# Performance work log

Measured on AMD Instinct MI355X. Metric: run time of the kernel, lower is better.

The kernel has to match this reference:

```python
import jax, jax.numpy as jnp
import numpy as np

NF = 32      # feature channels
DG = 4       # deformable groups
K = 9        # 3x3 kernel taps


def _conv(x, w, b, stride=1):
    # x: [B,C,H,W], w: [O,I,3,3] (pad=1)
    y = jax.lax.conv_general_dilated(x, w, (stride, stride), ((1, 1), (1, 1)),
                                     dimension_numbers=('NCHW', 'OIHW', 'NCHW'))
    return y + b[None, :, None, None]


def _lrelu(x):
    return jnp.where(x >= 0, x, 0.1 * x)


def _up2(x):
    # bilinear, align_corners=False (half-pixel centers, matches torch F.interpolate)
    B, C, H, W = x.shape
    return jax.image.resize(x, (B, C, 2 * H, 2 * W), method='bilinear')


def _deform_conv(x, om, w, b):
    # Modulated deformable conv (DCNv2), stride=1, pad=1, dilation=1, 3x3.
    # x: [B,C,H,W]; om: [B,3*DG*K,H,W] = (offset_y | offset_x | mask) blocks.
    B, C, H, W = x.shape
    Cg = C // DG
    o1, o2, m = jnp.split(om, 3, axis=1)
    off_y = o1.reshape(B, DG, K, H, W)
    off_x = o2.reshape(B, DG, K, H, W)
    mask = jax.nn.sigmoid(m).reshape(B, DG, K, H, W)
    k = jnp.arange(K)
    dy = (k // 3 - 1).astype(x.dtype)            # kernel tap y displacement
    dx = (k % 3 - 1).astype(x.dtype)
    # sampling positions [B,DG,K,H,W]
    py = off_y + jnp.arange(H, dtype=x.dtype)[:, None] + dy[:, None, None]
    px = off_x + jnp.arange(W, dtype=x.dtype)[None, :] + dx[:, None, None]
    y0 = jnp.floor(py)
    x0 = jnp.floor(px)
    wy1 = py - y0
    wx1 = px - x0
    y0i = y0.astype(jnp.int32)
    x0i = x0.astype(jnp.int32)
    imgf = x.reshape(B, DG, Cg, H * W)

    def corner(yi, xi, wt):
        valid = (yi >= 0) & (yi < H) & (xi >= 0) & (xi < W)
        yc = jnp.clip(yi, 0, H - 1)
        xc = jnp.clip(xi, 0, W - 1)
        idx = (yc * W + xc).reshape(B, DG, 1, K * H * W)
        v = jnp.take_along_axis(imgf, idx, axis=3).reshape(B, DG, Cg, K, H, W)
        return v * (wt * valid)[:, :, None]

    samp = (corner(y0i, x0i, (1 - wy1) * (1 - wx1))
            + corner(y0i, x0i + 1, (1 - wy1) * wx1)
            + corner(y0i + 1, x0i, wy1 * (1 - wx1))
            + corner(y0i + 1, x0i + 1, wy1 * wx1))
    samp = samp * mask[:, :, None]                       # [B,DG,Cg,K,H,W]
    out = jnp.einsum('bgckhw,ogck->bohw', samp, w.reshape(w.shape[0], DG, Cg, K))
    return out + b[None, :, None, None]


_PARAM_SHAPES = [
    ('w1_1', (32, 64, 3, 3)), ('b1_1', (32,)),
    ('w2_1', (32, 32, 3, 3)), ('b2_1', (32,)),
    ('w3_1', (32, 32, 3, 3)), ('b3_1', (32,)),
    ('w4_1', (32, 32, 3, 3)), ('b4_1', (32,)),
    ('w6_1', (32, 32, 3, 3)), ('b6_1', (32,)),
    ('w7_1', (32, 32, 3, 3)), ('b7_1', (32,)),
    ('w1_2', (32, 64, 3, 3)), ('b1_2', (32,)),
    ('w2_2', (32, 32, 3, 3)), ('b2_2', (32,)),
    ('w3_2', (32, 64, 3, 3)), ('b3_2', (32,)),
    ('w4_2', (32, 32, 3, 3)), ('b4_2', (32,)),
    ('w_om', (108, 32, 3, 3)), ('b_om', (108,)),   # DCN_sep conv_offset_mask: 3*DG*K=108
    ('w_dcn', (32, 32, 3, 3)), ('b_dcn', (32,)),
]


def setup_inputs() -> dict:
    key = jax.random.key(0)
    ks = jax.random.split(key, len(_PARAM_SHAPES) + 2)
    B, H, W = 4, 192, 192
    d = {
        'fea1': jax.random.normal(ks[0], (B, NF, H, W), jnp.float32),
        'fea2': jax.random.normal(ks[1], (B, NF, H, W), jnp.float32),
    }
    for i, (name, shp) in enumerate(_PARAM_SHAPES):
        d[name] = jax.random.normal(ks[i + 2], shp, jnp.float32) * 0.05
    return d


def reference(fea1, fea2, w1_1, b1_1, w2_1, b2_1, w3_1, b3_1, w4_1, b4_1,
              w6_1, b6_1, w7_1, b7_1, w1_2, b1_2, w2_2, b2_2, w3_2, b3_2,
              w4_2, b4_2, w_om, b_om, w_dcn, b_dcn):
    off = _lrelu(_conv(jnp.concatenate([fea1, fea2], 1), w1_1, b1_1))
    off1 = _lrelu(_conv(off, w2_1, b2_1))
    off2 = _lrelu(_conv(off1, w3_1, b3_1, 2))   # H/2
    off2 = _lrelu(_conv(off2, w4_1, b4_1))
    off3 = _lrelu(_conv(off2, w6_1, b6_1, 2))   # H/4
    off3 = _lrelu(_conv(off3, w7_1, b7_1))
    up = _up2(off3)                              # back to H/2
    off = _lrelu(_conv(jnp.concatenate([up, off2], 1), w1_2, b1_2))
    off = _lrelu(_conv(off, w2_2, b2_2))
    up = _up2(off)                               # back to H
    off = _lrelu(_conv(jnp.concatenate([up, off1], 1), w3_2, b3_2))
    base_offset = _conv(off, w4_2, b4_2)
    om = _conv(base_offset, w_om, b_om)          # DCN_sep offset/mask head
    return _deform_conv(fea2, om, w_dcn, b_dcn)
```

## Files before the change

kernel.cpp:

```cpp
#include <hip/hip_runtime.h>
#include <math.h>


#define BDIM 256

typedef __attribute__((ext_vector_type(8))) short short8v;
typedef __attribute__((ext_vector_type(4))) float f32x4;

__device__ __forceinline__ unsigned short f2bf(float f) {
    unsigned u = __builtin_bit_cast(unsigned, f);
    u = (u + 0x7FFF + ((u >> 16) & 1)) >> 16;
    return (unsigned short)u;
}
__device__ __forceinline__ float bf2f(unsigned short h) {
    unsigned u = ((unsigned)h) << 16;
    return __builtin_bit_cast(float, u);
}

template<int NPASS, int NHALF, int STRIDE, bool LRELU>
__global__ __launch_bounds__(BDIM, 4)
void convm_k(const short* __restrict__ in0, const short* __restrict__ in1,
             const short* __restrict__ wf,
             const float* __restrict__ bias,
             short* __restrict__ out,
             int Hin, int Win, int Hout, int Wout, int OCS)
{
    const int lane = threadIdx.x & 63;
    const int wid  = blockIdx.x * 4 + (threadIdx.x >> 6);
    const int segs = Wout >> 4;
    const int b  = wid / (Hout * segs);
    int r = wid - b * (Hout * segs);
    const int oy = r / segs;
    const int x0 = (r - oy * segs) * 16;
    const int lp = lane & 15;
    const int g  = lane >> 4;

    int rowOff[3]; bool rowOk[3];
#pragma unroll
    for (int ty = 0; ty < 3; ++ty) {
        const int iy = oy * STRIDE + ty - 1;
        rowOk[ty] = (unsigned)iy < (unsigned)Hin;
        rowOff[ty] = min(max(iy, 0), Hin - 1) * Win;
    }
    int colOff[3]; bool colOk[3];
#pragma unroll
    for (int tx = 0; tx < 3; ++tx) {
        const int ix = (x0 + lp) * STRIDE + tx - 1;
        colOk[tx] = (unsigned)ix < (unsigned)Win;
        colOff[tx] = min(max(ix, 0), Win - 1) * 32 + g * 8;
    }

    f32x4 acc[NHALF];
#pragma unroll
    for (int h = 0; h < NHALF; ++h) acc[h] = (f32x4){0.f, 0.f, 0.f, 0.f};

    const size_t inPlane = (size_t)Hin * Win * 32;
    const short8v zero = {};

#pragma unroll
    for (int pass = 0; pass < NPASS; ++pass) {
        const short* inp = (pass == 0 ? in0 : in1) + (size_t)b * inPlane;

        short8v bv[9];
#pragma unroll
        for (int t = 0; t < 9; ++t) {
            const int ty = t / 3, tx = t % 3;
            short8v v = *(const short8v*)(inp + (size_t)rowOff[ty] * 32 + colOff[tx]);
            bv[t] = (rowOk[ty] & colOk[tx]) ? v : zero;
        }
#pragma unroll
        for (int t = 0; t < 9; ++t) {
#pragma unroll
            for (int h = 0; h < NHALF; ++h) {
                short8v av = *(const short8v*)(
                    wf + ((((size_t)pass * 9 + t) * NHALF + h) * 64 + lane) * 8);
                acc[h] = __builtin_amdgcn_mfma_f32_16x16x32_bf16(av, bv[t], acc[h], 0, 0, 0);
            }
        }
    }

    short* op = out + (((size_t)b * Hout + oy) * Wout + x0 + lp) * OCS;
#pragma unroll
    for (int h = 0; h < NHALF; ++h) {
        const int co0 = h * 16 + g * 4;
        ushort4 st;
#pragma unroll
        for (int j = 0; j < 4; ++j) {
            float v = acc[h][j] + bias[co0 + j];
            if (LRELU) v = (v >= 0.f) ? v : 0.1f * v;
            ((unsigned short*)&st)[j] = f2bf(v);
        }
        *(ushort4*)(op + co0) = st;
    }
}

struct WPArgs {
    const float* src[11];
    int off[11];
    int npass[11], nhalf[11], O[11];
};

__global__ __launch_bounds__(BDIM)
void wprep_k(WPArgs a, short* __restrict__ wbase)
{
    const int z = blockIdx.z;
    const int n = a.npass[z] * 9 * a.nhalf[z] * 512;
    const int idx = blockIdx.x * BDIM + threadIdx.x;
    if (idx >= n) return;
    const int j = idx & 7;
    const int l = (idx >> 3) & 63;
    int r = idx >> 9;
    const int h = r % a.nhalf[z]; r /= a.nhalf[z];
    const int t = r % 9;
    const int pass = r / 9;
    const int I = a.npass[z] * 32;
    const int cout = h * 16 + (l & 15);
    const int cin  = pass * 32 + (l >> 4) * 8 + j;
    float v = (cout < a.O[z]) ? a.src[z][((size_t)cout * I + cin) * 9 + t] : 0.f;
    wbase[a.off[z] + idx] = (short)f2bf(v);
}

__global__ __launch_bounds__(BDIM)
void wdp_k(const float* __restrict__ w, short* __restrict__ dst)
{
    const int idx = blockIdx.x * BDIM + threadIdx.x;
    if (idx >= 9 * 2 * 64 * 8) return;
    const int j = idx & 7;
    const int l = (idx >> 3) & 63;
    const int h = (idx >> 9) & 1;
    const int k = idx >> 10;
    const int cout = h * 16 + (l & 15);
    const int cin  = (l >> 4) * 8 + j;
    dst[idx] = (short)f2bf(w[((size_t)cout * 32 + cin) * 9 + k]);
}

__global__ __launch_bounds__(BDIM)
void cvtnhwc_k(const float* __restrict__ s0, const float* __restrict__ s1,
               short* __restrict__ d0, short* __restrict__ d1, int H, int W)
{
    const float* s = blockIdx.z ? s1 : s0;
    short* d = blockIdx.z ? d1 : d0;
    const int idx = blockIdx.x * BDIM + threadIdx.x;
    if (idx >= 4 * 32 * H * W) return;
    const int c = idx & 31;
    int t = idx >> 5;
    const int x = t % W; t /= W;
    const int y = t % H;
    const int b = t / H;
    d[idx] = (short)f2bf(s[(((size_t)b * 32 + c) * H + y) * W + x]);
}

__global__ __launch_bounds__(BDIM)
void up2b_k(const short* __restrict__ in, short* __restrict__ out,
            int Hin, int Win)
{
    const int Hout = 2 * Hin, Wout = 2 * Win;
    const int idx = blockIdx.x * BDIM + threadIdx.x;
    if (idx >= 4 * Hout * Wout * 4) return;
    const int cg = idx & 3;
    int t = idx >> 2;
    const int x = t % Wout; t /= Wout;
    const int y = t % Hout;
    const int b = t / Hout;

    const float sy = (y + 0.5f) * 0.5f - 0.5f;
    const float sx = (x + 0.5f) * 0.5f - 0.5f;
    const float y0f = floorf(sy), x0f = floorf(sx);
    const float wy = sy - y0f, wx = sx - x0f;
    const int y0 = (int)y0f, x0 = (int)x0f;
    const int y0c = min(max(y0, 0), Hin - 1);
    const int y1c = min(max(y0 + 1, 0), Hin - 1);
    const int x0c = min(max(x0, 0), Win - 1);
    const int x1c = min(max(x0 + 1, 0), Win - 1);

    const short* base = in + (size_t)b * Hin * Win * 32 + cg * 8;
    short8v v00 = *(const short8v*)(base + ((size_t)y0c * Win + x0c) * 32);
    short8v v01 = *(const short8v*)(base + ((size_t)y0c * Win + x1c) * 32);
    short8v v10 = *(const short8v*)(base + ((size_t)y1c * Win + x0c) * 32);
    short8v v11 = *(const short8v*)(base + ((size_t)y1c * Win + x1c) * 32);

    short8v o;
#pragma unroll
    for (int j = 0; j < 8; ++j) {
        float f = (1.f - wy) * ((1.f - wx) * bf2f((unsigned short)v00[j]) +
                                wx * bf2f((unsigned short)v01[j]))
                + wy * ((1.f - wx) * bf2f((unsigned short)v10[j]) +
                        wx * bf2f((unsigned short)v11[j]));
        o[j] = (short)f2bf(f);
    }
    short* op = out + (size_t)b * Hout * Wout * 32 + ((size_t)y * Wout + x) * 32 + cg * 8;
    *(short8v*)op = o;
}

__global__ __launch_bounds__(BDIM, 4)
void dcnm_k(const short* __restrict__ xb,
            const short* __restrict__ bo,
            const short* __restrict__ wfo,
            const float* __restrict__ obias,
            const short* __restrict__ wfd,
            const float* __restrict__ bias,
            float* __restrict__ out, int H, int W)
{
    __shared__ unsigned short omld[4][16][112];

    const int lane = threadIdx.x & 63;
    const int wv   = threadIdx.x >> 6;
    const int wid  = blockIdx.x * 4 + wv;
    const int segs = W >> 4;
    const int b = wid / (H * segs);
    int r = wid - b * (H * segs);
    const int y = r / segs;
    const int x0 = (r - y * segs) * 16;
    const int lp = lane & 15;
    const int g  = lane >> 4;
    const int x  = x0 + lp;
    const size_t plane = (size_t)H * W;
    const short8v zero = {};

    {
        int rowOff[3]; bool rowOk[3];
#pragma unroll
        for (int ty = 0; ty < 3; ++ty) {
            const int iy = y + ty - 1;
            rowOk[ty] = (unsigned)iy < (unsigned)H;
            rowOff[ty] = min(max(iy, 0), H - 1) * W;
        }
        int colOff[3]; bool colOk[3];
#pragma unroll
        for (int tx = 0; tx < 3; ++tx) {
            const int ix = x + tx - 1;
            colOk[tx] = (unsigned)ix < (unsigned)W;
            colOff[tx] = min(max(ix, 0), W - 1) * 32 + g * 8;
        }
        const short* inp = bo + (size_t)b * plane * 32;
        short8v bv[9];
#pragma unroll
        for (int t = 0; t < 9; ++t) {
            const int ty = t / 3, tx = t % 3;
            short8v v = *(const short8v*)(inp + (size_t)rowOff[ty] * 32 + colOff[tx]);
            bv[t] = (rowOk[ty] & colOk[tx]) ? v : zero;
        }
        f32x4 acc[7];
#pragma unroll
        for (int h = 0; h < 7; ++h) acc[h] = (f32x4){0.f, 0.f, 0.f, 0.f};
#pragma unroll
        for (int t = 0; t < 9; ++t) {
#pragma unroll
            for (int h = 0; h < 7; ++h) {
                short8v av = *(const short8v*)(wfo + (((size_t)t * 7 + h) * 64 + lane) * 8);
                acc[h] = __builtin_amdgcn_mfma_f32_16x16x32_bf16(av, bv[t], acc[h], 0, 0, 0);
            }
        }
#pragma unroll
        for (int h = 0; h < 7; ++h) {
            const int co0 = h * 16 + g * 4;
            ushort4 st;
#pragma unroll
            for (int j = 0; j < 4; ++j)
                ((unsigned short*)&st)[j] = f2bf(acc[h][j] + obias[min(co0 + j, 107)]);
            *(ushort4*)&omld[wv][lp][co0] = st;
        }
    }
    __syncthreads();

    f32x4 p0 = (f32x4){0.f, 0.f, 0.f, 0.f};
    f32x4 p1 = (f32x4){0.f, 0.f, 0.f, 0.f};
    const short* xbb = xb + (size_t)b * plane * 32 + g * 8;

#pragma unroll
    for (int k = 0; k < 9; ++k) {
        const float offy = bf2f(omld[wv][lp][g * 9 + k]);
        const float offx = bf2f(omld[wv][lp][36 + g * 9 + k]);
        const float ml   = bf2f(omld[wv][lp][72 + g * 9 + k]);
        const float m = 1.f / (1.f + __expf(-ml));

        const float py = offy + (float)y + (float)(k / 3 - 1);
        const float px = offx + (float)x + (float)(k % 3 - 1);
        const float y0f = floorf(py), x0f = floorf(px);
        const int y0 = (int)y0f, x0i = (int)x0f;
        const float wy1 = py - y0f, wx1 = px - x0f;
        const float wy0 = 1.f - wy1, wx0 = 1.f - wx1;

        const bool y0ok = (unsigned)y0 < (unsigned)H;
        const bool y1ok = (unsigned)(y0 + 1) < (unsigned)H;
        const bool x0ok = (unsigned)x0i < (unsigned)W;
        const bool x1ok = (unsigned)(x0i + 1) < (unsigned)W;
        const int y0c = min(max(y0, 0), H - 1);
        const int y1c = min(max(y0 + 1, 0), H - 1);
        const int x0c = min(max(x0i, 0), W - 1);
        const int x1c = min(max(x0i + 1, 0), W - 1);

        const float w00 = wy0 * wx0 * ((y0ok && x0ok) ? 1.f : 0.f) * m;
        const float w01 = wy0 * wx1 * ((y0ok && x1ok) ? 1.f : 0.f) * m;
        const float w10 = wy1 * wx0 * ((y1ok && x0ok) ? 1.f : 0.f) * m;
        const float w11 = wy1 * wx1 * ((y1ok && x1ok) ? 1.f : 0.f) * m;

        short8v v00 = *(const short8v*)(xbb + ((size_t)y0c * W + x0c) * 32);
        short8v v01 = *(const short8v*)(xbb + ((size_t)y0c * W + x1c) * 32);
        short8v v10 = *(const short8v*)(xbb + ((size_t)y1c * W + x0c) * 32);
        short8v v11 = *(const short8v*)(xbb + ((size_t)y1c * W + x1c) * 32);

        short8v bv;
#pragma unroll
        for (int j = 0; j < 8; ++j) {
            float s = w00 * bf2f((unsigned short)v00[j])
                    + w01 * bf2f((unsigned short)v01[j])
                    + w10 * bf2f((unsigned short)v10[j])
                    + w11 * bf2f((unsigned short)v11[j]);
            bv[j] = (short)f2bf(s);
        }

        short8v a0 = *(const short8v*)(wfd + (((size_t)k * 2 + 0) * 64 + lane) * 8);
        short8v a1 = *(const short8v*)(wfd + (((size_t)k * 2 + 1) * 64 + lane) * 8);
        p0 = __builtin_amdgcn_mfma_f32_16x16x32_bf16(a0, bv, p0, 0, 0, 0);
        p1 = __builtin_amdgcn_mfma_f32_16x16x32_bf16(a1, bv, p1, 0, 0, 0);
    }

    float* op = out + (size_t)b * 32 * plane + (size_t)y * W + x;
#pragma unroll
    for (int j = 0; j < 4; ++j) {
        const int co0 = g * 4 + j;
        const int co1 = 16 + g * 4 + j;
        op[(size_t)co0 * plane] = p0[j] + bias[co0];
        op[(size_t)co1 * plane] = p1[j] + bias[co1];
    }
}


extern "C" void kernel_launch(void* const* d_in, const int* in_sizes, int n_in,
                              void* d_out, int out_size, void* d_ws, size_t ws_size,
                              hipStream_t stream)
{
    const float* fea1  = (const float*)d_in[0];
    const float* fea2  = (const float*)d_in[1];
    const float* w1_1  = (const float*)d_in[2];  const float* b1_1 = (const float*)d_in[3];
    const float* w2_1  = (const float*)d_in[4];  const float* b2_1 = (const float*)d_in[5];
    const float* w3_1  = (const float*)d_in[6];  const float* b3_1 = (const float*)d_in[7];
    const float* w4_1  = (const float*)d_in[8];  const float* b4_1 = (const float*)d_in[9];
    const float* w6_1  = (const float*)d_in[10]; const float* b6_1 = (const float*)d_in[11];
    const float* w7_1  = (const float*)d_in[12]; const float* b7_1 = (const float*)d_in[13];
    const float* w1_2  = (const float*)d_in[14]; const float* b1_2 = (const float*)d_in[15];
    const float* w2_2  = (const float*)d_in[16]; const float* b2_2 = (const float*)d_in[17];
    const float* w3_2  = (const float*)d_in[18]; const float* b3_2 = (const float*)d_in[19];
    const float* w4_2  = (const float*)d_in[20]; const float* b4_2 = (const float*)d_in[21];
    const float* w_om  = (const float*)d_in[22]; const float* b_om = (const float*)d_in[23];
    const float* w_dcn = (const float*)d_in[24]; const float* b_dcn= (const float*)d_in[25];

    const int H = 192, W = 192;
    char* ws = (char*)d_ws;

    short* fea1b = (short*)(ws + 0);
    short* fea2b = (short*)(ws + 9437184);
    short* bufA  = (short*)(ws + 18874368);
    short* bufB  = (short*)(ws + 28311552);
    short* bufC  = (short*)(ws + 0);
    short* bufD  = (short*)(ws + 2359296);
    short* bufE  = (short*)(ws + 4718592);
    short* bufF  = (short*)(ws + 5308416);
    short* bufG  = (short*)(ws + 5898240);
    short* bufH  = (short*)(ws + 0);
    short* bufI  = (short*)(ws + 4718592);
    short* bufJ  = (short*)(ws + 37748736);
    short* bufK  = (short*)(ws + 18874368);
    short* bufL  = (short*)(ws + 0);
    short* wfrag = (short*)(ws + 70778880);
    short* wfdcn = (short*)(ws + 71083008);

    const int WOFF[11] = {0, 18432, 27648, 36864, 46080, 55296,
                          64512, 82944, 92160, 110592, 119808};

    dim3 blk(BDIM, 1, 1);

    {
        WPArgs a;
        const float* srcs[11] = {w1_1, w2_1, w3_1, w4_1, w6_1, w7_1,
                                 w1_2, w2_2, w3_2, w4_2, w_om};
        const int NP[11] = {2,1,1,1,1,1,2,1,2,1,1};
        const int NH[11] = {2,2,2,2,2,2,2,2,2,2,7};
        const int Os[11] = {32,32,32,32,32,32,32,32,32,32,108};
        for (int i = 0; i < 11; ++i) {
            a.src[i] = srcs[i]; a.off[i] = WOFF[i];
            a.npass[i] = NP[i]; a.nhalf[i] = NH[i]; a.O[i] = Os[i];
        }
        wprep_k<<<dim3(126, 1, 11), blk, 0, stream>>>(a, wfrag);
        cvtnhwc_k<<<dim3(18432, 1, 2), blk, 0, stream>>>(fea1, fea2, fea1b, fea2b, H, W);
        wdp_k<<<dim3(36), blk, 0, stream>>>(w_dcn, wfdcn);
    }

    convm_k<2,2,1,true><<<dim3(2304), blk, 0, stream>>>(
        fea1b, fea2b, wfrag + WOFF[0], b1_1, bufA, 192,192,192,192, 32);
    convm_k<1,2,1,true><<<dim3(2304), blk, 0, stream>>>(
        bufA, nullptr, wfrag + WOFF[1], b2_1, bufB, 192,192,192,192, 32);
    convm_k<1,2,2,true><<<dim3(576), blk, 0, stream>>>(
        bufB, nullptr, wfrag + WOFF[2], b3_1, bufC, 192,192,96,96, 32);
    convm_k<1,2,1,true><<<dim3(576), blk, 0, stream>>>(
        bufC, nullptr, wfrag + WOFF[3], b4_1, bufD, 96,96,96,96, 32);
    convm_k<1,2,2,true><<<dim3(144), blk, 0, stream>>>(
        bufD, nullptr, wfrag + WOFF[4], b6_1, bufE, 96,96,48,48, 32);
    convm_k<1,2,1,true><<<dim3(144), blk, 0, stream>>>(
        bufE, nullptr, wfrag + WOFF[5], b7_1, bufF, 48,48,48,48, 32);
    up2b_k<<<dim3(576), blk, 0, stream>>>(bufF, bufG, 48, 48);
    convm_k<2,2,1,true><<<dim3(576), blk, 0, stream>>>(
        bufG, bufD, wfrag + WOFF[6], b1_2, bufH, 96,96,96,96, 32);
    convm_k<1,2,1,true><<<dim3(576), blk, 0, stream>>>(
        bufH, nullptr, wfrag + WOFF[7], b2_2, bufI, 96,96,96,96, 32);
    up2b_k<<<dim3(2304), blk, 0, stream>>>(bufI, bufJ, 96, 96);
    convm_k<2,2,1,true><<<dim3(2304), blk, 0, stream>>>(
        bufJ, bufB, wfrag + WOFF[8], b3_2, bufK, 192,192,192,192, 32);
    convm_k<1,2,1,false><<<dim3(2304), blk, 0, stream>>>(
        bufK, nullptr, wfrag + WOFF[9], b4_2, bufL, 192,192,192,192, 32);
    dcnm_k<<<dim3(2304), blk, 0, stream>>>(
        fea2b, bufL, wfrag + WOFF[10], b_om, wfdcn, b_dcn, (float*)d_out, H, W);
}
```

Before: 325.1 us.

## Add row-strip conv kernel with rolling register window for full-res layers

```diff
diff --git a/kernel.cpp b/kernel.cpp
--- a/kernel.cpp
+++ b/kernel.cpp
@@ -15,6 +15,117 @@
 __device__ __forceinline__ float bf2f(unsigned short h) {
     unsigned u = ((unsigned)h) << 16;
     return __builtin_bit_cast(float, u);
+}
+
+template<int NPASS, bool LRELU, int YS>
+__global__ __launch_bounds__(BDIM, 2)
+void convr_k(const short* __restrict__ in0, const short* __restrict__ in1,
+             const short* __restrict__ wf,
+             const float* __restrict__ bias,
+             short* __restrict__ out, int H, int W)
+{
+    const int lane = threadIdx.x & 63;
+    const int wid  = blockIdx.x * 4 + (threadIdx.x >> 6);
+    const int segs = W >> 4;
+    const int strips = (H / YS) * segs;
+    const int b = wid / strips;
+    int r = wid - b * strips;
+    const int ys = r / segs;
+    const int y0 = ys * YS;
+    const int x0 = (r - ys * segs) * 16;
+    const int lp = lane & 15;
+    const int g  = lane >> 4;
+
+    int colOff[3]; bool colOk[3];
+#pragma unroll
+    for (int tx = 0; tx < 3; ++tx) {
+        const int ix = x0 + lp + tx - 1;
+        colOk[tx] = (unsigned)ix < (unsigned)W;
+        colOff[tx] = min(max(ix, 0), W - 1) * 32 + g * 8;
+    }
+
+    const size_t inPlane = (size_t)H * W * 32;
+    const short8v zero = {};
+    const short* inp0 = in0 + (size_t)b * inPlane;
+    const short* inp1 = (NPASS > 1) ? in1 + (size_t)b * inPlane : nullptr;
+
+    short8v awc[(NPASS == 1) ? 18 : 1];
+    if constexpr (NPASS == 1) {
+#pragma unroll
+        for (int t = 0; t < 9; ++t)
+#pragma unroll
+            for (int h = 0; h < 2; ++h)
+                awc[t * 2 + h] = *(const short8v*)(
+                    wf + (((size_t)t * 2 + h) * 64 + lane) * 8);
+    }
+
+    short8v win[NPASS][3][3];
+
+#define LOADROW(SLOT, IY) do {                                                \
+        const int iy_ = (IY);                                                 \
+        const bool rok_ = (unsigned)iy_ < (unsigned)H;                        \
+        const int ro_ = min(max(iy_, 0), H - 1) * W;                          \
+        _Pragma("unroll")                                                     \
+        for (int tx = 0; tx < 3; ++tx) {                                      \
+            short8v v_ = *(const short8v*)(inp0 + (size_t)ro_ * 32 + colOff[tx]); \
+            win[0][SLOT][tx] = (rok_ & colOk[tx]) ? v_ : zero;                \
+            if constexpr (NPASS > 1) {                                        \
+                short8v w_ = *(const short8v*)(inp1 + (size_t)ro_ * 32 + colOff[tx]); \
+                win[1][SLOT][tx] = (rok_ & colOk[tx]) ? w_ : zero;            \
+            }                                                                 \
+        }                                                                     \
+    } while (0)
+
+    LOADROW(0, y0 - 1);
+    LOADROW(1, y0);
+
+#pragma unroll
+    for (int s = 0; s < YS; ++s) {
+        LOADROW((s + 2) % 3, y0 + s + 1);
+
+        f32x4 a0 = (f32x4){0.f, 0.f, 0.f, 0.f};
+        f32x4 a1 = (f32x4){0.f, 0.f, 0.f, 0.f};
+#pragma unroll
+        for (int p = 0; p < NPASS; ++p) {
+#pragma unroll
+            for (int ty = 0; ty < 3; ++ty) {
+#pragma unroll
+                for (int tx = 0; tx < 3; ++tx) {
+                    const int t = ty * 3 + tx;
+                    const short8v bv = win[p][(s + ty) % 3][tx];
+                    short8v av0, av1;
+                    if constexpr (NPASS == 1) {
+                        av0 = awc[t * 2 + 0];
+                        av1 = awc[t * 2 + 1];
+                    } else {
+                        av0 = *(const short8v*)(
+                            wf + ((((size_t)p * 9 + t) * 2 + 0) * 64 + lane) * 8);
+                        av1 = *(const short8v*)(
+                            wf + ((((size_t)p * 9 + t) * 2 + 1) * 64 + lane) * 8);
+                    }
+                    a0 = __builtin_amdgcn_mfma_f32_16x16x32_bf16(av0, bv, a0, 0, 0, 0);
+                    a1 = __builtin_amdgcn_mfma_f32_16x16x32_bf16(av1, bv, a1, 0, 0, 0);
+                }
+            }
+        }
+
+        short* op = out + (((size_t)b * H + (y0 + s)) * W + x0 + lp) * 32;
+        ushort4 st0, st1;
+#pragma unroll
+        for (int j = 0; j < 4; ++j) {
+            float v0 = a0[j] + bias[g * 4 + j];
+            float v1 = a1[j] + bias[16 + g * 4 + j];
+            if (LRELU) {
+                v0 = (v0 >= 0.f) ? v0 : 0.1f * v0;
+                v1 = (v1 >= 0.f) ? v1 : 0.1f * v1;
+            }
+            ((unsigned short*)&st0)[j] = f2bf(v0);
+            ((unsigned short*)&st1)[j] = f2bf(v1);
+        }
+        *(ushort4*)(op + g * 4) = st0;
+        *(ushort4*)(op + 16 + g * 4) = st1;
+    }
+#undef LOADROW
 }
 
 template<int NPASS, int NHALF, int STRIDE, bool LRELU>
@@ -261,7 +372,6 @@
             *(ushort4*)&omld[wv][lp][co0] = st;
         }
     }
-    __syncthreads();
 
     f32x4 p0 = (f32x4){0.f, 0.f, 0.f, 0.f};
     f32x4 p1 = (f32x4){0.f, 0.f, 0.f, 0.f};
@@ -387,10 +497,10 @@
         wdp_k<<<dim3(36), blk, 0, stream>>>(w_dcn, wfdcn);
     }
 
-    convm_k<2,2,1,true><<<dim3(2304), blk, 0, stream>>>(
-        fea1b, fea2b, wfrag + WOFF[0], b1_1, bufA, 192,192,192,192, 32);
-    convm_k<1,2,1,true><<<dim3(2304), blk, 0, stream>>>(
-        bufA, nullptr, wfrag + WOFF[1], b2_1, bufB, 192,192,192,192, 32);
+    convr_k<2,true,4><<<dim3(576), blk, 0, stream>>>(
+        fea1b, fea2b, wfrag + WOFF[0], b1_1, bufA, 192, 192);
+    convr_k<1,true,4><<<dim3(576), blk, 0, stream>>>(
+        bufA, nullptr, wfrag + WOFF[1], b2_1, bufB, 192, 192);
     convm_k<1,2,2,true><<<dim3(576), blk, 0, stream>>>(
         bufB, nullptr, wfrag + WOFF[2], b3_1, bufC, 192,192,96,96, 32);
     convm_k<1,2,1,true><<<dim3(576), blk, 0, stream>>>(
@@ -405,10 +515,10 @@
     convm_k<1,2,1,true><<<dim3(576), blk, 0, stream>>>(
         bufH, nullptr, wfrag + WOFF[7], b2_2, bufI, 96,96,96,96, 32);
     up2b_k<<<dim3(2304), blk, 0, stream>>>(bufI, bufJ, 96, 96);
-    convm_k<2,2,1,true><<<dim3(2304), blk, 0, stream>>>(
-        bufJ, bufB, wfrag + WOFF[8], b3_2, bufK, 192,192,192,192, 32);
-    convm_k<1,2,1,false><<<dim3(2304), blk, 0, stream>>>(
-        bufK, nullptr, wfrag + WOFF[9], b4_2, bufL, 192,192,192,192, 32);
+    convr_k<2,true,4><<<dim3(576), blk, 0, stream>>>(
+        bufJ, bufB, wfrag + WOFF[8], b3_2, bufK, 192, 192);
+    convr_k<1,false,4><<<dim3(576), blk, 0, stream>>>(
+        bufK, nullptr, wfrag + WOFF[9], b4_2, bufL, 192, 192);
     dcnm_k<<<dim3(2304), blk, 0, stream>>>(
         fea2b, bufL, wfrag + WOFF[10], b_om, wfdcn, b_dcn, (float*)d_out, H, W);
 }
```

After: 313.3 us. 3.6% less time.
